# Performance work log

Hardware: AMD Instinct MI355X
Metric: run time of the kernel (lower is better)

Reference implementation:

```python
import jax, jax.numpy as jnp
import numpy as np

NUM_NODES = 50000
NUM_EDGES = 800000
NUM_GRAPHS = 100
NODES_PER_GRAPH = 500
K = 250  # ceil(0.5 * NODES_PER_GRAPH), TopKPooling ratio=0.5
D = 64
OUT = 10


def gcn_conv(x, edge_index, W, b, num_nodes):
    """PyG GCNConv: add self-loops, symmetric D^-1/2 (A+I) D^-1/2 (x @ W) + b."""
    h = x @ W  # [N, Dout]
    loop = jnp.arange(num_nodes)
    row = jnp.concatenate([edge_index[0], loop])  # sources
    col = jnp.concatenate([edge_index[1], loop])  # targets
    deg = jax.ops.segment_sum(jnp.ones_like(col, dtype=h.dtype), col,
                              num_segments=num_nodes)
    dis = jnp.where(deg > 0, jax.lax.rsqrt(jnp.maximum(deg, 1e-12)), 0.0)
    norm = dis[row] * dis[col]                      # [E+N]
    msgs = h[row] * norm[:, None]                   # gather + scale (memory bound)
    out = jax.ops.segment_sum(msgs, col, num_segments=num_nodes)
    return out + b


def setup_inputs() -> dict:
    key = jax.random.key(0)
    ks = jax.random.split(key, 8)
    x = jax.random.normal(ks[0], (NUM_NODES, D), jnp.float32)
    edge_index = jax.random.randint(ks[1], (2, NUM_EDGES), 0, NUM_NODES)
    batch = jnp.arange(NUM_NODES) // NODES_PER_GRAPH  # contiguous equal graphs
    s = 1.0 / np.sqrt(D)
    W0 = jax.random.uniform(ks[2], (D, D), jnp.float32, -s, s)
    b0 = jnp.zeros((D,), jnp.float32)
    W1 = jax.random.uniform(ks[3], (D, D), jnp.float32, -s, s)
    b1 = jnp.zeros((D,), jnp.float32)
    pool_w = jax.random.uniform(ks[4], (D,), jnp.float32, -s, s)
    W_lin = jax.random.uniform(ks[5], (D, OUT), jnp.float32, -s, s)
    b_lin = jnp.zeros((OUT,), jnp.float32)
    return {"x": x, "edge_index": edge_index, "batch": batch,
            "W0": W0, "b0": b0, "W1": W1, "b1": b1,
            "pool_w": pool_w, "W_lin": W_lin, "b_lin": b_lin}


def reference(x, edge_index, batch, W0, b0, W1, b1, pool_w, W_lin, b_lin):
    # NOTE: zip(convs, pools) runs only 2 iterations -> 2 convs, 1 pool.
    x = jax.nn.relu(gcn_conv(x, edge_index, W0, b0, NUM_NODES))
    x = jax.nn.relu(gcn_conv(x, edge_index, W1, b1, NUM_NODES))
    # TopKPooling: score = tanh((x . w) / ||w||), keep top-K per graph,
    # kept features are scaled by their score.
    score = jnp.tanh((x @ pool_w) / jnp.linalg.norm(pool_w))  # [N]
    score_g = score.reshape(NUM_GRAPHS, NODES_PER_GRAPH)
    top_s, top_i = jax.lax.top_k(score_g, K)                  # [G, K]
    gidx = (top_i + jnp.arange(NUM_GRAPHS)[:, None] * NODES_PER_GRAPH).reshape(-1)
    x_pool = x[gidx] * top_s.reshape(-1, 1)                   # [G*K, D]
    # global_mean_pool: each pooled graph has exactly K nodes
    pooled = x_pool.reshape(NUM_GRAPHS, K, D).mean(axis=1)    # [G, D]
    logits = pooled @ W_lin + b_lin                           # [G, OUT]
    return jax.nn.log_softmax(logits, axis=1)
```

## Files before the change

### kernel.cpp

```cpp
#include <hip/hip_runtime.h>
#include <hip/hip_bf16.h>
#include <math.h>

#define NODES 50000
#define EDGES 800000
#define GRAPHS 100
#define NPG 500
#define KTOP 250
#define DIM 64
#define OUTC 10
#define SLOTS 64
#define GROWS 32
#define NBKT 196
#define BCAP 5120

#define WS_FLAG      0u
#define WS_INVNORM   4u
#define WS_W1F       512u
#define WS_B0F       16896u
#define WS_B1F       17152u
#define WS_PWF       17408u
#define WS_WLF       17664u
#define WS_BLF       20224u
#define WS_CURS      20480u
#define WS_CNT       21504u
#define WS_DIS       221696u
#define WS_SCORE     421888u
#define WS_EBUF      622080u
#define WS_SLOT      4636160u
#define WS_H1B       11036160u
#define WS_H2B       17436160u
#define WS_X2        23836160u

__device__ __forceinline__ float bf16_bits_to_f32(unsigned short u) {
    return __uint_as_float(((unsigned int)u) << 16);
}
__device__ __forceinline__ float bf16_lo(unsigned int u) {
    return __uint_as_float(u << 16);
}
__device__ __forceinline__ float bf16_hi(unsigned int u) {
    return __uint_as_float(u & 0xffff0000u);
}
__device__ __forceinline__ unsigned short f32_to_bf16(float f) {
    unsigned int u = __float_as_uint(f);
    u += 0x7fffu + ((u >> 16) & 1u);
    return (unsigned short)(u >> 16);
}
__device__ __forceinline__ unsigned int f32_sortable(float f) {
    unsigned int b = __float_as_uint(f);
    return (b & 0x80000000u) ? ~b : (b | 0x80000000u);
}

__global__ __launch_bounds__(512) void k_bucket(const int* __restrict__ ei,
        const void* w0p, const void* b0p, const void* w1p, const void* b1p,
        const void* pwp, const void* wlp, const void* blp, char* __restrict__ ws) {
    int bid = blockIdx.x, t = threadIdx.x;
    if (bid < NBKT) {
        __shared__ int hist[NBKT];
        __shared__ int base[NBKT];
        if (t < NBKT) hist[t] = 0;
        __syncthreads();
        int e0 = bid * 4096;
        int rr[8], cc[8], loc[8];
        long be = (long)e0 + (long)t * 8;
        if (be + 8 <= EDGES) {
            int4 ra = ((const int4*)(ei + e0))[t * 2];
            int4 rb = ((const int4*)(ei + e0))[t * 2 + 1];
            int4 ca = ((const int4*)(ei + EDGES + e0))[t * 2];
            int4 cb = ((const int4*)(ei + EDGES + e0))[t * 2 + 1];
            rr[0] = ra.x; rr[1] = ra.y; rr[2] = ra.z; rr[3] = ra.w;
            rr[4] = rb.x; rr[5] = rb.y; rr[6] = rb.z; rr[7] = rb.w;
            cc[0] = ca.x; cc[1] = ca.y; cc[2] = ca.z; cc[3] = ca.w;
            cc[4] = cb.x; cc[5] = cb.y; cc[6] = cb.z; cc[7] = cb.w;
        } else {
#pragma unroll
            for (int j = 0; j < 8; j++) {
                long e = be + j;
                if (e < EDGES) { rr[j] = ei[e]; cc[j] = ei[EDGES + e]; }
                else cc[j] = -1;
            }
        }
#pragma unroll
        for (int j = 0; j < 8; j++)
            if (cc[j] >= 0) loc[j] = atomicAdd(&hist[cc[j] >> 8], 1);
        __syncthreads();
        if (t < NBKT) base[t] = atomicAdd((int*)(ws + WS_CURS) + t, hist[t]);
        __syncthreads();
        unsigned int* eb = (unsigned int*)(ws + WS_EBUF);
#pragma unroll
        for (int j = 0; j < 8; j++) {
            if (cc[j] >= 0) {
                int b = cc[j] >> 8;
                int o = base[b] + loc[j];
                if (o < BCAP)
                    eb[b * BCAP + o] =
                        ((unsigned int)(cc[j] & 255) << 16) | (unsigned int)rr[j];
            }
        }
        return;
    }
    __shared__ int red_sh[512];
    __shared__ float fred[64];
    const unsigned short* u16 = (const unsigned short*)w0p;
    int c = 0;
    for (int i = t; i < 4096; i += 512) {
        float v = bf16_bits_to_f32(u16[i]);
        float av = fabsf(v);
        if (v == 0.0f || (av >= 1e-9f && av <= 0.25f)) c++;
    }
    red_sh[t] = c;
    __syncthreads();
    for (int s = 256; s > 0; s >>= 1) {
        if (t < s) red_sh[t] += red_sh[t + s];
        __syncthreads();
    }
    int flag = (red_sh[0] >= 3686) ? 1 : 0;
    if (t == 0) *(int*)(ws + WS_FLAG) = flag;
    const void* srcs[6] = {w1p, b0p, b1p, pwp, wlp, blp};
    const int   ns[6]   = {4096, 64, 64, 64, 640, 10};
    const unsigned int dsts[6] = {WS_W1F, WS_B0F, WS_B1F, WS_PWF, WS_WLF, WS_BLF};
    for (int a = 0; a < 6; a++) {
        float* dst = (float*)(ws + dsts[a]);
        if (flag) {
            const unsigned short* sp = (const unsigned short*)srcs[a];
            for (int i = t; i < ns[a]; i += 512) dst[i] = bf16_bits_to_f32(sp[i]);
        } else {
            const float* sp = (const float*)srcs[a];
            for (int i = t; i < ns[a]; i += 512) dst[i] = sp[i];
        }
    }
    __syncthreads();
    if (t < 64) {
        float w = ((float*)(ws + WS_PWF))[t];
        fred[t] = w * w;
    }
    __syncthreads();
    if (t == 0) {
        float ssum = 0.f;
        for (int i = 0; i < 64; i++) ssum += fred[i];
        *(float*)(ws + WS_INVNORM) = rsqrtf(ssum);
    }
}

__global__ __launch_bounds__(1024) void k_build(char* __restrict__ ws) {
    __shared__ unsigned short slsh[256 * SLOTS];
    __shared__ int cl_cnt[256];
    int b = blockIdx.x, t = threadIdx.x;
    if (t < 256) cl_cnt[t] = 0;
    __syncthreads();
    int n = ((const int*)(ws + WS_CURS))[b];
    if (n > BCAP) n = BCAP;
    const unsigned int* eb = (const unsigned int*)(ws + WS_EBUF) + b * BCAP;
    for (int i = t; i < n; i += 1024) {
        unsigned int u = eb[i];
        int cl = u >> 16;
        int r = u & 0xffffu;
        int p = atomicAdd(&cl_cnt[cl], 1);
        if (p < SLOTS) slsh[cl * SLOTS + p] = (unsigned short)r;
    }
    __syncthreads();
    uint4* dstv = (uint4*)((unsigned short*)(ws + WS_SLOT) + (b << 8) * SLOTS);
    const uint4* srcv = (const uint4*)slsh;
    for (int i = t; i < 2048; i += 1024) dstv[i] = srcv[i];
    if (t < 256) {
        int v = (b << 8) + t;
        if (v < NODES) {
            int cv = cl_cnt[t];
            ((int*)(ws + WS_CNT))[v] = cv;
            ((float*)(ws + WS_DIS))[v] = rsqrtf((float)(cv + 1));
        }
    }
}

__global__ __launch_bounds__(256) void k_gemm0(const void* __restrict__ xp,
        const void* __restrict__ w0p, char* __restrict__ ws,
        unsigned short* __restrict__ H1B) {
    __shared__ float Wsh[64 * 64];
    __shared__ float xsh[GROWS * 65];
    int bid = blockIdx.x, t = threadIdx.x;
    int flag = *(const int*)(ws + WS_FLAG);
    if (flag) {
        const unsigned short* wp = (const unsigned short*)w0p;
        for (int i = t; i < 4096; i += 256) Wsh[i] = bf16_bits_to_f32(wp[i]);
    } else {
        for (int i = t; i < 1024; i += 256)
            ((float4*)Wsh)[i] = ((const float4*)w0p)[i];
    }
    int row0 = bid * GROWS;
    for (int i = t; i < GROWS * 16; i += 256) {
        int r = i >> 4, q = i & 15;
        int gr = row0 + r;
        float4 v = {0.f, 0.f, 0.f, 0.f};
        if (gr < NODES) {
            if (flag) {
                ushort4 u = ((const ushort4*)xp)[gr * 16 + q];
                v.x = bf16_bits_to_f32(u.x); v.y = bf16_bits_to_f32(u.y);
                v.z = bf16_bits_to_f32(u.z); v.w = bf16_bits_to_f32(u.w);
            } else {
                v = ((const float4*)xp)[gr * 16 + q];
            }
        }
        float* xd = xsh + r * 65 + q * 4;
        xd[0] = v.x; xd[1] = v.y; xd[2] = v.z; xd[3] = v.w;
    }
    __syncthreads();
    int tc = t & 15, tr = t >> 4;
    int c0 = tc * 4, r0 = tr * 2;
    float4 a0 = {0, 0, 0, 0}, a1 = {0, 0, 0, 0};
#pragma unroll
    for (int k = 0; k < 64; k++) {
        float4 wv = *(const float4*)(Wsh + k * 64 + c0);
        float x0 = xsh[r0 * 65 + k];
        float x1 = xsh[(r0 + 1) * 65 + k];
        a0.x += wv.x * x0; a0.y += wv.y * x0; a0.z += wv.z * x0; a0.w += wv.w * x0;
        a1.x += wv.x * x1; a1.y += wv.y * x1; a1.z += wv.z * x1; a1.w += wv.w * x1;
    }
    int gr0 = row0 + r0;
    const float* dis = (const float*)(ws + WS_DIS);
    if (gr0 < NODES) {
        float d0 = dis[gr0];
        ushort4 s0;
        s0.x = f32_to_bf16(a0.x * d0); s0.y = f32_to_bf16(a0.y * d0);
        s0.z = f32_to_bf16(a0.z * d0); s0.w = f32_to_bf16(a0.w * d0);
        *(ushort4*)(H1B + gr0 * 64 + c0) = s0;
    }
    if (gr0 + 1 < NODES) {
        float d1 = dis[gr0 + 1];
        ushort4 s1;
        s1.x = f32_to_bf16(a1.x * d1); s1.y = f32_to_bf16(a1.y * d1);
        s1.z = f32_to_bf16(a1.z * d1); s1.w = f32_to_bf16(a1.w * d1);
        *(ushort4*)(H1B + (gr0 + 1) * 64 + c0) = s1;
    }
}

__device__ __forceinline__ void agg_core(const unsigned short* __restrict__ HB,
        const char* __restrict__ ws, int v, int eg, int dh,
        const float* bias, float4& olo, float4& ohi, float& dvo) {
    const int* cnt = (const int*)(ws + WS_CNT);
    const unsigned short* slot = (const unsigned short*)(ws + WS_SLOT) + v * SLOTS;
    const float* dis = (const float*)(ws + WS_DIS);
    int deg = cnt[v];
    if (deg > SLOTS) deg = SLOTS;
    float dv = dis[v];
    dvo = dv;
    float4 alo = {0, 0, 0, 0}, ahi = {0, 0, 0, 0};
    float4 blo = {0, 0, 0, 0}, bhi = {0, 0, 0, 0};
    if (eg == 0) {
        uint4 u = *(const uint4*)(HB + v * 64 + dh * 8);
        alo.x = bf16_lo(u.x); alo.y = bf16_hi(u.x);
        alo.z = bf16_lo(u.y); alo.w = bf16_hi(u.y);
        ahi.x = bf16_lo(u.z); ahi.y = bf16_hi(u.z);
        ahi.z = bf16_lo(u.w); ahi.w = bf16_hi(u.w);
    }
    int e = eg;
    for (; e + 8 < deg; e += 16) {
        int sA = slot[e], sB = slot[e + 8];
        uint4 uA = *(const uint4*)(HB + sA * 64 + dh * 8);
        uint4 uB = *(const uint4*)(HB + sB * 64 + dh * 8);
        alo.x += bf16_lo(uA.x); alo.y += bf16_hi(uA.x);
        alo.z += bf16_lo(uA.y); alo.w += bf16_hi(uA.y);
        ahi.x += bf16_lo(uA.z); ahi.y += bf16_hi(uA.z);
        ahi.z += bf16_lo(uA.w); ahi.w += bf16_hi(uA.w);
        blo.x += bf16_lo(uB.x); blo.y += bf16_hi(uB.x);
        blo.z += bf16_lo(uB.y); blo.w += bf16_hi(uB.y);
        bhi.x += bf16_lo(uB.z); bhi.y += bf16_hi(uB.z);
        bhi.z += bf16_lo(uB.w); bhi.w += bf16_hi(uB.w);
    }
    if (e < deg) {
        int sA = slot[e];
        uint4 uA = *(const uint4*)(HB + sA * 64 + dh * 8);
        alo.x += bf16_lo(uA.x); alo.y += bf16_hi(uA.x);
        alo.z += bf16_lo(uA.y); alo.w += bf16_hi(uA.y);
        ahi.x += bf16_lo(uA.z); ahi.y += bf16_hi(uA.z);
        ahi.z += bf16_lo(uA.w); ahi.w += bf16_hi(uA.w);
    }
    alo.x += blo.x; alo.y += blo.y; alo.z += blo.z; alo.w += blo.w;
    ahi.x += bhi.x; ahi.y += bhi.y; ahi.z += bhi.z; ahi.w += bhi.w;
#pragma unroll
    for (int m = 8; m <= 32; m <<= 1) {
        alo.x += __shfl_xor(alo.x, m, 64); alo.y += __shfl_xor(alo.y, m, 64);
        alo.z += __shfl_xor(alo.z, m, 64); alo.w += __shfl_xor(alo.w, m, 64);
        ahi.x += __shfl_xor(ahi.x, m, 64); ahi.y += __shfl_xor(ahi.y, m, 64);
        ahi.z += __shfl_xor(ahi.z, m, 64); ahi.w += __shfl_xor(ahi.w, m, 64);
    }
    float4 b4a = *(const float4*)(bias + dh * 8);
    float4 b4b = *(const float4*)(bias + dh * 8 + 4);
    olo.x = fmaxf(alo.x * dv + b4a.x, 0.f);
    olo.y = fmaxf(alo.y * dv + b4a.y, 0.f);
    olo.z = fmaxf(alo.z * dv + b4a.z, 0.f);
    olo.w = fmaxf(alo.w * dv + b4a.w, 0.f);
    ohi.x = fmaxf(ahi.x * dv + b4b.x, 0.f);
    ohi.y = fmaxf(ahi.y * dv + b4b.y, 0.f);
    ohi.z = fmaxf(ahi.z * dv + b4b.z, 0.f);
    ohi.w = fmaxf(ahi.w * dv + b4b.w, 0.f);
}

__global__ __launch_bounds__(512) void k_agg1g(const unsigned short* __restrict__ H1B,
        char* __restrict__ ws, unsigned short* __restrict__ H2B) {
    __shared__ float Wsh[4096];
    int t = threadIdx.x;
    const float* W1F = (const float*)(ws + WS_W1F);
    for (int i = t; i < 4096; i += 512) {
        int k = i >> 6, cc = i & 63;
        int qp = (cc >> 2) ^ (k >> 3);
        Wsh[k * 64 + (qp << 2) + (cc & 3)] = W1F[i];
    }
    __syncthreads();
    int wv = t >> 6, lane = t & 63, eg = lane >> 3, dh = lane & 7;
    int v = blockIdx.x * 8 + wv;
    float4 olo, ohi;
    float dv;
    agg_core(H1B, ws, v, eg, dh, (const float*)(ws + WS_B0F), olo, ohi, dv);
    float av[8] = {olo.x, olo.y, olo.z, olo.w, ohi.x, ohi.y, ohi.z, ohi.w};
    float y[8] = {0.f, 0.f, 0.f, 0.f, 0.f, 0.f, 0.f, 0.f};
    const float* Wk = Wsh + dh * 512;
    int q0 = (((eg << 1)) ^ dh) << 2;
    int q1 = (((eg << 1) | 1) ^ dh) << 2;
#pragma unroll
    for (int j = 0; j < 8; j++) {
        float a = av[j];
        float4 w0 = *(const float4*)(Wk + j * 64 + q0);
        float4 w1 = *(const float4*)(Wk + j * 64 + q1);
        y[0] += a * w0.x; y[1] += a * w0.y; y[2] += a * w0.z; y[3] += a * w0.w;
        y[4] += a * w1.x; y[5] += a * w1.y; y[6] += a * w1.z; y[7] += a * w1.w;
    }
#pragma unroll
    for (int m = 1; m <= 4; m <<= 1) {
#pragma unroll
        for (int q = 0; q < 8; q++) y[q] += __shfl_xor(y[q], m, 64);
    }
    if (dh < 2) {
        ushort4 s;
        if (dh == 0) {
            s.x = f32_to_bf16(y[0] * dv); s.y = f32_to_bf16(y[1] * dv);
            s.z = f32_to_bf16(y[2] * dv); s.w = f32_to_bf16(y[3] * dv);
        } else {
            s.x = f32_to_bf16(y[4] * dv); s.y = f32_to_bf16(y[5] * dv);
            s.z = f32_to_bf16(y[6] * dv); s.w = f32_to_bf16(y[7] * dv);
        }
        *(ushort4*)(H2B + v * 64 + (eg << 3) + (dh << 2)) = s;
    }
}

__global__ __launch_bounds__(256) void k_agg_sc(const unsigned short* __restrict__ H2B,
        char* __restrict__ ws, float* __restrict__ X2) {
    int t = threadIdx.x;
    int wv = t >> 6, lane = t & 63, eg = lane >> 3, dh = lane & 7;
    int v = blockIdx.x * 4 + wv;
    float4 olo, ohi;
    float dv;
    agg_core(H2B, ws, v, eg, dh, (const float*)(ws + WS_B1F), olo, ohi, dv);
    if (lane < 8) {
        *(float4*)(X2 + v * 64 + lane * 8) = olo;
        *(float4*)(X2 + v * 64 + lane * 8 + 4) = ohi;
    }
    const float* pw = (const float*)(ws + WS_PWF);
    float4 p4a = *(const float4*)(pw + dh * 8);
    float4 p4b = *(const float4*)(pw + dh * 8 + 4);
    float p = olo.x * p4a.x + olo.y * p4a.y + olo.z * p4a.z + olo.w * p4a.w
            + ohi.x * p4b.x + ohi.y * p4b.y + ohi.z * p4b.z + ohi.w * p4b.w;
    p += __shfl_xor(p, 1, 64);
    p += __shfl_xor(p, 2, 64);
    p += __shfl_xor(p, 4, 64);
    if (lane == 0) {
        float invn = *(const float*)(ws + WS_INVNORM);
        ((float*)(ws + WS_SCORE))[v] = tanhf(p * invn);
    }
}

template<int K, int J>
__device__ __forceinline__ void bstage(unsigned long long (&a)[8], int lane) {
    if constexpr (J >= 8) {
        constexpr int m = J >> 3;
#pragma unroll
        for (int s = 0; s < 8; s++) {
            unsigned long long other = __shfl_xor(a[s], m, 64);
            int e = (lane << 3) | s;
            bool keep_min = ((e & K) == 0) ^ ((lane & m) != 0);
            bool less = a[s] < other;
            a[s] = (keep_min == less) ? a[s] : other;
        }
    } else {
#pragma unroll
        for (int s = 0; s < 8; s++) {
            if ((s & J) == 0) {
                constexpr int j = J;
                int sp = s | j;
                int e = (lane << 3) | s;
                bool up = ((e & K) == 0);
                bool sw = up ? (a[s] > a[sp]) : (a[s] < a[sp]);
                if (sw) { unsigned long long tmp = a[s]; a[s] = a[sp]; a[sp] = tmp; }
            }
        }
    }
    if constexpr (J > 1) bstage<K, (J >> 1)>(a, lane);
}

__global__ __launch_bounds__(256) void k_topk(char* __restrict__ ws,
        const float* __restrict__ X2, void* __restrict__ out) {
    __shared__ unsigned long long pairs[KTOP];
    __shared__ float part[256];
    __shared__ float pool_sh[64];
    __shared__ float lsh[OUTC];
    int g = blockIdx.x, t = threadIdx.x;
    int wv = t >> 6, lane = t & 63;
    const float* sc = (const float*)(ws + WS_SCORE) + g * NPG;

    if (wv == 0) {
        unsigned long long a[8];
#pragma unroll
        for (int s = 0; s < 8; s++) {
            int e = (lane << 3) | s;
            if (e < NPG) {
                unsigned int key = ~f32_sortable(sc[e]);
                a[s] = ((unsigned long long)key << 32) | (unsigned int)e;
            } else {
                a[s] = 0xFFFFFFFFFFFFFFFFull;
            }
        }
        bstage<2, 1>(a, lane);
        bstage<4, 2>(a, lane);
        bstage<8, 4>(a, lane);
        bstage<16, 8>(a, lane);
        bstage<32, 16>(a, lane);
        bstage<64, 32>(a, lane);
        bstage<128, 64>(a, lane);
        bstage<256, 128>(a, lane);
        bstage<512, 256>(a, lane);
#pragma unroll
        for (int s = 0; s < 8; s++) {
            int r = (lane << 3) | s;
            if (r < KTOP) pairs[r] = a[s];
        }
    }
    __syncthreads();

    int d = lane;
    float acc = 0.f;
    for (int r = wv; r < KTOP; r += 4) {
        unsigned long long p = pairs[r];
        unsigned int u = ~(unsigned int)(p >> 32);
        unsigned int sbits = (u & 0x80000000u) ? (u ^ 0x80000000u) : ~u;
        float score = __uint_as_float(sbits);
        int idx = (int)(p & 0xFFFFFFFFu);
        acc += score * X2[(g * NPG + idx) * 64 + d];
    }
    part[t] = acc;
    __syncthreads();
    if (wv == 0)
        pool_sh[d] = (part[d] + part[64 + d] + part[128 + d] + part[192 + d]) * (1.0f / KTOP);
    __syncthreads();
    if (t < 64) {
        float pd = pool_sh[t];
        const float* Wl = (const float*)(ws + WS_WLF);
        const float* bl = (const float*)(ws + WS_BLF);
        for (int o = 0; o < OUTC; o++) {
            float p = pd * Wl[t * OUTC + o];
            for (int s = 32; s > 0; s >>= 1) p += __shfl_down(p, s, 64);
            if (t == 0) lsh[o] = p + bl[o];
        }
        if (t == 0) {
            int flag = *(const int*)(ws + WS_FLAG);
            float mx = lsh[0];
            for (int o = 1; o < OUTC; o++) mx = fmaxf(mx, lsh[o]);
            float se = 0.f;
            for (int o = 0; o < OUTC; o++) se += expf(lsh[o] - mx);
            float lse = logf(se);
            for (int o = 0; o < OUTC; o++) {
                float vv = lsh[o] - mx - lse;
                if (flag) ((__hip_bfloat16*)out)[g * OUTC + o] = __float2bfloat16(vv);
                else      ((float*)out)[g * OUTC + o] = vv;
            }
        }
    }
}

extern "C" void kernel_launch(void* const* d_in, const int* in_sizes, int n_in,
                              void* d_out, int out_size, void* d_ws, size_t ws_size,
                              hipStream_t stream) {
    (void)in_sizes; (void)n_in; (void)out_size; (void)ws_size;
    char* ws = (char*)d_ws;
    const void* xp = d_in[0];
    const int* ei = (const int*)d_in[1];
    unsigned short* H1B = (unsigned short*)(ws + WS_H1B);
    unsigned short* H2B = (unsigned short*)(ws + WS_H2B);
    float* X2 = (float*)(ws + WS_X2);

    (void)hipMemsetAsync(ws + WS_CURS, 0, NBKT * sizeof(int), stream);
    k_bucket<<<NBKT + 1, 512, 0, stream>>>(ei, d_in[3], d_in[4], d_in[5],
                                           d_in[6], d_in[7], d_in[8], d_in[9], ws);
    k_build<<<NBKT, 1024, 0, stream>>>(ws);
    k_gemm0<<<1563, 256, 0, stream>>>(xp, d_in[3], ws, H1B);
    k_agg1g<<<6250, 512, 0, stream>>>(H1B, ws, H2B);
    k_agg_sc<<<12500, 256, 0, stream>>>(H2B, ws, X2);
    k_topk<<<100, 256, 0, stream>>>(ws, X2, d_out);
}
```

Baseline: 158.3 us.

## Remap second aggregation to eight threads per node with serial edge loop

The second GCN aggregation kernel is rewritten so that each node is handled by 8 lanes, each owning 8 feature columns, instead of a full 64-lane wavefront. Each lane walks the node's neighbor slot list sequentially, two edges at a time with dual accumulators. This drops the cross-lane shuffle reductions and the idle lanes of the old per-wave scheme. In exchange each thread runs a serial dependent loop over up to 64 neighbors, so memory-level parallelism per node falls and load imbalance from varying degrees grows.

Measured after the change: 152.1 us. -3.9%, faster.

```diff
diff --git a/kernel.cpp b/kernel.cpp
--- a/kernel.cpp
+++ b/kernel.cpp
@@ -342,27 +342,69 @@
     }
 }
 
-__global__ __launch_bounds__(256) void k_agg_sc(const unsigned short* __restrict__ H2B,
+__global__ __launch_bounds__(256) void k_agg2(const unsigned short* __restrict__ H2B,
         char* __restrict__ ws, float* __restrict__ X2) {
     int t = threadIdx.x;
-    int wv = t >> 6, lane = t & 63, eg = lane >> 3, dh = lane & 7;
-    int v = blockIdx.x * 4 + wv;
-    float4 olo, ohi;
-    float dv;
-    agg_core(H2B, ws, v, eg, dh, (const float*)(ws + WS_B1F), olo, ohi, dv);
-    if (lane < 8) {
-        *(float4*)(X2 + v * 64 + lane * 8) = olo;
-        *(float4*)(X2 + v * 64 + lane * 8 + 4) = ohi;
-    }
-    const float* pw = (const float*)(ws + WS_PWF);
-    float4 p4a = *(const float4*)(pw + dh * 8);
-    float4 p4b = *(const float4*)(pw + dh * 8 + 4);
-    float p = olo.x * p4a.x + olo.y * p4a.y + olo.z * p4a.z + olo.w * p4a.w
-            + ohi.x * p4b.x + ohi.y * p4b.y + ohi.z * p4b.z + ohi.w * p4b.w;
+    int g = t >> 3, dl = t & 7;
+    int v = blockIdx.x * 32 + g;
+    if (v >= NODES) return;
+    int deg = ((const int*)(ws + WS_CNT))[v];
+    if (deg > SLOTS) deg = SLOTS;
+    float dv = ((const float*)(ws + WS_DIS))[v];
+    const unsigned short* slot = (const unsigned short*)(ws + WS_SLOT) + v * SLOTS;
+    const unsigned short* rb = H2B + dl * 8;
+    uint4 u = *(const uint4*)(rb + v * 64);
+    float a0 = bf16_lo(u.x), a1 = bf16_hi(u.x), a2 = bf16_lo(u.y), a3 = bf16_hi(u.y);
+    float a4 = bf16_lo(u.z), a5 = bf16_hi(u.z), a6 = bf16_lo(u.w), a7 = bf16_hi(u.w);
+    float b0 = 0.f, b1 = 0.f, b2 = 0.f, b3 = 0.f;
+    float b4 = 0.f, b5 = 0.f, b6 = 0.f, b7 = 0.f;
+    int e = 0;
+    for (; e + 1 < deg; e += 2) {
+        int sA = slot[e], sB = slot[e + 1];
+        uint4 uA = *(const uint4*)(rb + sA * 64);
+        uint4 uB = *(const uint4*)(rb + sB * 64);
+        a0 += bf16_lo(uA.x); a1 += bf16_hi(uA.x);
+        a2 += bf16_lo(uA.y); a3 += bf16_hi(uA.y);
+        a4 += bf16_lo(uA.z); a5 += bf16_hi(uA.z);
+        a6 += bf16_lo(uA.w); a7 += bf16_hi(uA.w);
+        b0 += bf16_lo(uB.x); b1 += bf16_hi(uB.x);
+        b2 += bf16_lo(uB.y); b3 += bf16_hi(uB.y);
+        b4 += bf16_lo(uB.z); b5 += bf16_hi(uB.z);
+        b6 += bf16_lo(uB.w); b7 += bf16_hi(uB.w);
+    }
+    if (e < deg) {
+        int sA = slot[e];
+        uint4 uA = *(const uint4*)(rb + sA * 64);
+        a0 += bf16_lo(uA.x); a1 += bf16_hi(uA.x);
+        a2 += bf16_lo(uA.y); a3 += bf16_hi(uA.y);
+        a4 += bf16_lo(uA.z); a5 += bf16_hi(uA.z);
+        a6 += bf16_lo(uA.w); a7 += bf16_hi(uA.w);
+    }
+    a0 += b0; a1 += b1; a2 += b2; a3 += b3;
+    a4 += b4; a5 += b5; a6 += b6; a7 += b7;
+    const float* bias = (const float*)(ws + WS_B1F) + dl * 8;
+    float4 bb0 = *(const float4*)(bias);
+    float4 bb1 = *(const float4*)(bias + 4);
+    float4 o0, o1;
+    o0.x = fmaxf(a0 * dv + bb0.x, 0.f);
+    o0.y = fmaxf(a1 * dv + bb0.y, 0.f);
+    o0.z = fmaxf(a2 * dv + bb0.z, 0.f);
+    o0.w = fmaxf(a3 * dv + bb0.w, 0.f);
+    o1.x = fmaxf(a4 * dv + bb1.x, 0.f);
+    o1.y = fmaxf(a5 * dv + bb1.y, 0.f);
+    o1.z = fmaxf(a6 * dv + bb1.z, 0.f);
+    o1.w = fmaxf(a7 * dv + bb1.w, 0.f);
+    *(float4*)(X2 + v * 64 + dl * 8) = o0;
+    *(float4*)(X2 + v * 64 + dl * 8 + 4) = o1;
+    const float* pw = (const float*)(ws + WS_PWF) + dl * 8;
+    float4 pa = *(const float4*)(pw);
+    float4 pb = *(const float4*)(pw + 4);
+    float p = o0.x * pa.x + o0.y * pa.y + o0.z * pa.z + o0.w * pa.w
+            + o1.x * pb.x + o1.y * pb.y + o1.z * pb.z + o1.w * pb.w;
     p += __shfl_xor(p, 1, 64);
     p += __shfl_xor(p, 2, 64);
     p += __shfl_xor(p, 4, 64);
-    if (lane == 0) {
+    if (dl == 0) {
         float invn = *(const float*)(ws + WS_INVNORM);
         ((float*)(ws + WS_SCORE))[v] = tanhf(p * invn);
     }
@@ -492,6 +534,6 @@
     k_build<<<NBKT, 1024, 0, stream>>>(ws);
     k_gemm0<<<1563, 256, 0, stream>>>(xp, d_in[3], ws, H1B);
     k_agg1g<<<6250, 512, 0, stream>>>(H1B, ws, H2B);
-    k_agg_sc<<<12500, 256, 0, stream>>>(H2B, ws, X2);
+    k_agg2<<<1563, 256, 0, stream>>>(H2B, ws, X2);
     k_topk<<<100, 256, 0, stream>>>(ws, X2, d_out);
 }
```

## Split feature halves into separate buffers and aggregate each half in its own pass

Applied to the files above, without the earlier changes.

Node feature tables are stored as two 32-column bf16 halves, and each GCN aggregation runs as two launches, one per half. The goal is a smaller gather working set per pass so it fits better in cache. The second layer's transform, previously fused into the first aggregation, becomes a separate GEMM kernel over an intermediate bf16 activation buffer. The score dot product is split across the halves, with the partial sum kept in scratch. The cost is more launches and an extra write and read of the intermediate activations.

New measurement: 173.1 us. 9.4% more time.

```diff
diff --git a/kernel.cpp b/kernel.cpp
--- a/kernel.cpp
+++ b/kernel.cpp
@@ -13,6 +13,9 @@
 #define GROWS 32
 #define NBKT 196
 #define BCAP 5120
+
+typedef unsigned int nuint4 __attribute__((ext_vector_type(4)));
+typedef float nfloat4 __attribute__((ext_vector_type(4)));
 
 #define WS_FLAG      0u
 #define WS_INVNORM   4u
@@ -28,9 +31,14 @@
 #define WS_SCORE     421888u
 #define WS_EBUF      622080u
 #define WS_SLOT      4636160u
-#define WS_H1B       11036160u
-#define WS_H2B       17436160u
+#define WS_H1LO      11036160u
+#define WS_H1HI      14236160u
+#define WS_H2LO      17436160u
+#define WS_H2HI      20636160u
 #define WS_X2        23836160u
+#define WS_A1LO      WS_X2
+#define WS_A1HI      27036160u
+#define WS_PLO       WS_EBUF
 
 __device__ __forceinline__ float bf16_bits_to_f32(unsigned short u) {
     return __uint_as_float(((unsigned int)u) << 16);
@@ -46,9 +54,18 @@
     u += 0x7fffu + ((u >> 16) & 1u);
     return (unsigned short)(u >> 16);
 }
+__device__ __forceinline__ unsigned int pack_bf16x2(float lo, float hi) {
+    return ((unsigned int)f32_to_bf16(hi) << 16) | (unsigned int)f32_to_bf16(lo);
+}
 __device__ __forceinline__ unsigned int f32_sortable(float f) {
     unsigned int b = __float_as_uint(f);
     return (b & 0x80000000u) ? ~b : (b | 0x80000000u);
+}
+__device__ __forceinline__ void acc8(const uint4& u, float* a) {
+    a[0] += bf16_lo(u.x); a[1] += bf16_hi(u.x);
+    a[2] += bf16_lo(u.y); a[3] += bf16_hi(u.y);
+    a[4] += bf16_lo(u.z); a[5] += bf16_hi(u.z);
+    a[6] += bf16_lo(u.w); a[7] += bf16_hi(u.w);
 }
 
 __global__ __launch_bounds__(512) void k_bucket(const int* __restrict__ ei,
@@ -174,7 +191,7 @@
 
 __global__ __launch_bounds__(256) void k_gemm0(const void* __restrict__ xp,
         const void* __restrict__ w0p, char* __restrict__ ws,
-        unsigned short* __restrict__ H1B) {
+        unsigned short* __restrict__ H1LO, unsigned short* __restrict__ H1HI) {
     __shared__ float Wsh[64 * 64];
     __shared__ float xsh[GROWS * 65];
     int bid = blockIdx.x, t = threadIdx.x;
@@ -222,149 +239,184 @@
         ushort4 s0;
         s0.x = f32_to_bf16(a0.x * d0); s0.y = f32_to_bf16(a0.y * d0);
         s0.z = f32_to_bf16(a0.z * d0); s0.w = f32_to_bf16(a0.w * d0);
-        *(ushort4*)(H1B + gr0 * 64 + c0) = s0;
+        unsigned short* dst = (c0 < 32) ? (H1LO + gr0 * 32 + c0)
+                                        : (H1HI + gr0 * 32 + (c0 - 32));
+        *(ushort4*)dst = s0;
     }
     if (gr0 + 1 < NODES) {
         float d1 = dis[gr0 + 1];
         ushort4 s1;
         s1.x = f32_to_bf16(a1.x * d1); s1.y = f32_to_bf16(a1.y * d1);
         s1.z = f32_to_bf16(a1.z * d1); s1.w = f32_to_bf16(a1.w * d1);
-        *(ushort4*)(H1B + (gr0 + 1) * 64 + c0) = s1;
-    }
-}
-
-__device__ __forceinline__ void agg_core(const unsigned short* __restrict__ HB,
-        const char* __restrict__ ws, int v, int eg, int dh,
-        const float* bias, float4& olo, float4& ohi, float& dvo) {
-    const int* cnt = (const int*)(ws + WS_CNT);
+        unsigned short* dst = (c0 < 32) ? (H1LO + (gr0 + 1) * 32 + c0)
+                                        : (H1HI + (gr0 + 1) * 32 + (c0 - 32));
+        *(ushort4*)dst = s1;
+    }
+}
+
+__global__ __launch_bounds__(256) void k_agg1h(const unsigned short* __restrict__ Hh,
+        char* __restrict__ ws, unsigned short* __restrict__ A1h, int half) {
+    int t = threadIdx.x;
+    int g = t >> 3, l8 = t & 7, eg = l8 >> 2, dl = l8 & 3;
+    int v = blockIdx.x * 32 + g;
+    if (v >= NODES) return;
+    int deg = ((const int*)(ws + WS_CNT))[v];
+    if (deg > SLOTS) deg = SLOTS;
+    float dv = ((const float*)(ws + WS_DIS))[v];
     const unsigned short* slot = (const unsigned short*)(ws + WS_SLOT) + v * SLOTS;
+    const unsigned short* rb = Hh + dl * 8;
+    float a[8] = {0, 0, 0, 0, 0, 0, 0, 0};
+    float b[8] = {0, 0, 0, 0, 0, 0, 0, 0};
+    if (eg == 0) {
+        uint4 u = *(const uint4*)(rb + v * 32);
+        acc8(u, a);
+    }
+    int e = eg;
+    for (; e + 2 < deg; e += 4) {
+        int sA = slot[e], sB = slot[e + 2];
+        uint4 uA = *(const uint4*)(rb + sA * 32);
+        uint4 uB = *(const uint4*)(rb + sB * 32);
+        acc8(uA, a); acc8(uB, b);
+    }
+    if (e < deg) {
+        uint4 uA = *(const uint4*)(rb + slot[e] * 32);
+        acc8(uA, a);
+    }
+#pragma unroll
+    for (int j = 0; j < 8; j++) {
+        a[j] += b[j];
+        a[j] += __shfl_xor(a[j], 4, 64);
+    }
+    const float* bias = (const float*)(ws + WS_B0F) + half * 32 + dl * 8;
+    float o[8];
+#pragma unroll
+    for (int j = 0; j < 8; j++) o[j] = fmaxf(a[j] * dv + bias[j], 0.f);
+    if (eg == 0) {
+        nuint4 s;
+        s.x = pack_bf16x2(o[0], o[1]); s.y = pack_bf16x2(o[2], o[3]);
+        s.z = pack_bf16x2(o[4], o[5]); s.w = pack_bf16x2(o[6], o[7]);
+        __builtin_nontemporal_store(s, (nuint4*)(A1h + v * 32 + dl * 8));
+    }
+}
+
+__global__ __launch_bounds__(256) void k_gemm1(char* __restrict__ ws,
+        unsigned short* __restrict__ H2LO, unsigned short* __restrict__ H2HI) {
+    __shared__ float Wsh[64 * 64];
+    __shared__ float xsh[GROWS * 65];
+    int bid = blockIdx.x, t = threadIdx.x;
+    const float* W1F = (const float*)(ws + WS_W1F);
+    for (int i = t; i < 1024; i += 256)
+        ((float4*)Wsh)[i] = ((const float4*)W1F)[i];
+    const unsigned short* A1LO = (const unsigned short*)(ws + WS_A1LO);
+    const unsigned short* A1HI = (const unsigned short*)(ws + WS_A1HI);
+    int row0 = bid * GROWS;
+    for (int i = t; i < GROWS * 16; i += 256) {
+        int r = i >> 4, q = i & 15;
+        int gr = row0 + r;
+        int cc = q * 4;
+        float4 vv = {0.f, 0.f, 0.f, 0.f};
+        if (gr < NODES) {
+            const unsigned short* src = (cc < 32) ? (A1LO + gr * 32 + cc)
+                                                  : (A1HI + gr * 32 + (cc - 32));
+            ushort4 u = *(const ushort4*)src;
+            vv.x = bf16_bits_to_f32(u.x); vv.y = bf16_bits_to_f32(u.y);
+            vv.z = bf16_bits_to_f32(u.z); vv.w = bf16_bits_to_f32(u.w);
+        }
+        float* xd = xsh + r * 65 + cc;
+        xd[0] = vv.x; xd[1] = vv.y; xd[2] = vv.z; xd[3] = vv.w;
+    }
+    __syncthreads();
+    int tc = t & 15, tr = t >> 4;
+    int c0 = tc * 4, r0 = tr * 2;
+    float4 a0 = {0, 0, 0, 0}, a1 = {0, 0, 0, 0};
+#pragma unroll
+    for (int k = 0; k < 64; k++) {
+        float4 wv = *(const float4*)(Wsh + k * 64 + c0);
+        float x0 = xsh[r0 * 65 + k];
+        float x1 = xsh[(r0 + 1) * 65 + k];
+        a0.x += wv.x * x0; a0.y += wv.y * x0; a0.z += wv.z * x0; a0.w += wv.w * x0;
+        a1.x += wv.x * x1; a1.y += wv.y * x1; a1.z += wv.z * x1; a1.w += wv.w * x1;
+    }
+    int gr0 = row0 + r0;
     const float* dis = (const float*)(ws + WS_DIS);
-    int deg = cnt[v];
+    if (gr0 < NODES) {
+        float d = dis[gr0];
+        ushort4 s;
+        s.x = f32_to_bf16(a0.x * d); s.y = f32_to_bf16(a0.y * d);
+        s.z = f32_to_bf16(a0.z * d); s.w = f32_to_bf16(a0.w * d);
+        unsigned short* dst = (c0 < 32) ? (H2LO + gr0 * 32 + c0)
+                                        : (H2HI + gr0 * 32 + (c0 - 32));
+        *(ushort4*)dst = s;
+    }
+    if (gr0 + 1 < NODES) {
+        float d = dis[gr0 + 1];
+        ushort4 s;
+        s.x = f32_to_bf16(a1.x * d); s.y = f32_to_bf16(a1.y * d);
+        s.z = f32_to_bf16(a1.z * d); s.w = f32_to_bf16(a1.w * d);
+        unsigned short* dst = (c0 < 32) ? (H2LO + (gr0 + 1) * 32 + c0)
+                                        : (H2HI + (gr0 + 1) * 32 + (c0 - 32));
+        *(ushort4*)dst = s;
+    }
+}
+
+__global__ __launch_bounds__(256) void k_agg2h(const unsigned short* __restrict__ Hh,
+        char* __restrict__ ws, float* __restrict__ X2, int half) {
+    int t = threadIdx.x;
+    int g = t >> 3, l8 = t & 7, eg = l8 >> 2, dl = l8 & 3;
+    int v = blockIdx.x * 32 + g;
+    if (v >= NODES) return;
+    int deg = ((const int*)(ws + WS_CNT))[v];
     if (deg > SLOTS) deg = SLOTS;
-    float dv = dis[v];
-    dvo = dv;
-    float4 alo = {0, 0, 0, 0}, ahi = {0, 0, 0, 0};
-    float4 blo = {0, 0, 0, 0}, bhi = {0, 0, 0, 0};
+    float dv = ((const float*)(ws + WS_DIS))[v];
+    const unsigned short* slot = (const unsigned short*)(ws + WS_SLOT) + v * SLOTS;
+    const unsigned short* rb = Hh + dl * 8;
+    float a[8] = {0, 0, 0, 0, 0, 0, 0, 0};
+    float b[8] = {0, 0, 0, 0, 0, 0, 0, 0};
     if (eg == 0) {
-        uint4 u = *(const uint4*)(HB + v * 64 + dh * 8);
-        alo.x = bf16_lo(u.x); alo.y = bf16_hi(u.x);
-        alo.z = bf16_lo(u.y); alo.w = bf16_hi(u.y);
-        ahi.x = bf16_lo(u.z); ahi.y = bf16_hi(u.z);
-        ahi.z = bf16_lo(u.w); ahi.w = bf16_hi(u.w);
+        uint4 u = *(const uint4*)(rb + v * 32);
+        acc8(u, a);
     }
     int e = eg;
-    for (; e + 8 < deg; e += 16) {
-        int sA = slot[e], sB = slot[e + 8];
-        uint4 uA = *(const uint4*)(HB + sA * 64 + dh * 8);
-        uint4 uB = *(const uint4*)(HB + sB * 64 + dh * 8);
-        alo.x += bf16_lo(uA.x); alo.y += bf16_hi(uA.x);
-        alo.z += bf16_lo(uA.y); alo.w += bf16_hi(uA.y);
-        ahi.x += bf16_lo(uA.z); ahi.y += bf16_hi(uA.z);
-        ahi.z += bf16_lo(uA.w); ahi.w += bf16_hi(uA.w);
-        blo.x += bf16_lo(uB.x); blo.y += bf16_hi(uB.x);
-        blo.z += bf16_lo(uB.y); blo.w += bf16_hi(uB.y);
-        bhi.x += bf16_lo(uB.z); bhi.y += bf16_hi(uB.z);
-        bhi.z += bf16_lo(uB.w); bhi.w += bf16_hi(uB.w);
+    for (; e + 2 < deg; e += 4) {
+        int sA = slot[e], sB = slot[e + 2];
+        uint4 uA = *(const uint4*)(rb + sA * 32);
+        uint4 uB = *(const uint4*)(rb + sB * 32);
+        acc8(uA, a); acc8(uB, b);
     }
     if (e < deg) {
-        int sA = slot[e];
-        uint4 uA = *(const uint4*)(HB + sA * 64 + dh * 8);
-        alo.x += bf16_lo(uA.x); alo.y += bf16_hi(uA.x);
-        alo.z += bf16_lo(uA.y); alo.w += bf16_hi(uA.y);
-        ahi.x += bf16_lo(uA.z); ahi.y += bf16_hi(uA.z);
-        ahi.z += bf16_lo(uA.w); ahi.w += bf16_hi(uA.w);
-    }
-    alo.x += blo.x; alo.y += blo.y; alo.z += blo.z; alo.w += blo.w;
-    ahi.x += bhi.x; ahi.y += bhi.y; ahi.z += bhi.z; ahi.w += bhi.w;
-#pragma unroll
-    for (int m = 8; m <= 32; m <<= 1) {
-        alo.x += __shfl_xor(alo.x, m, 64); alo.y += __shfl_xor(alo.y, m, 64);
-        alo.z += __shfl_xor(alo.z, m, 64); alo.w += __shfl_xor(alo.w, m, 64);
-        ahi.x += __shfl_xor(ahi.x, m, 64); ahi.y += __shfl_xor(ahi.y, m, 64);
-        ahi.z += __shfl_xor(ahi.z, m, 64); ahi.w += __shfl_xor(ahi.w, m, 64);
-    }
-    float4 b4a = *(const float4*)(bias + dh * 8);
-    float4 b4b = *(const float4*)(bias + dh * 8 + 4);
-    olo.x = fmaxf(alo.x * dv + b4a.x, 0.f);
-    olo.y = fmaxf(alo.y * dv + b4a.y, 0.f);
-    olo.z = fmaxf(alo.z * dv + b4a.z, 0.f);
-    olo.w = fmaxf(alo.w * dv + b4a.w, 0.f);
-    ohi.x = fmaxf(ahi.x * dv + b4b.x, 0.f);
-    ohi.y = fmaxf(ahi.y * dv + b4b.y, 0.f);
-    ohi.z = fmaxf(ahi.z * dv + b4b.z, 0.f);
-    ohi.w = fmaxf(ahi.w * dv + b4b.w, 0.f);
-}
-
-__global__ __launch_bounds__(512) void k_agg1g(const unsigned short* __restrict__ H1B,
-        char* __restrict__ ws, unsigned short* __restrict__ H2B) {
-    __shared__ float Wsh[4096];
-    int t = threadIdx.x;
-    const float* W1F = (const float*)(ws + WS_W1F);
-    for (int i = t; i < 4096; i += 512) {
-        int k = i >> 6, cc = i & 63;
-        int qp = (cc >> 2) ^ (k >> 3);
-        Wsh[k * 64 + (qp << 2) + (cc & 3)] = W1F[i];
-    }
-    __syncthreads();
-    int wv = t >> 6, lane = t & 63, eg = lane >> 3, dh = lane & 7;
-    int v = blockIdx.x * 8 + wv;
-    float4 olo, ohi;
-    float dv;
-    agg_core(H1B, ws, v, eg, dh, (const float*)(ws + WS_B0F), olo, ohi, dv);
-    float av[8] = {olo.x, olo.y, olo.z, olo.w, ohi.x, ohi.y, ohi.z, ohi.w};
-    float y[8] = {0.f, 0.f, 0.f, 0.f, 0.f, 0.f, 0.f, 0.f};
-    const float* Wk = Wsh + dh * 512;
-    int q0 = (((eg << 1)) ^ dh) << 2;
-    int q1 = (((eg << 1) | 1) ^ dh) << 2;
+        uint4 uA = *(const uint4*)(rb + slot[e] * 32);
+        acc8(uA, a);
+    }
 #pragma unroll
     for (int j = 0; j < 8; j++) {
-        float a = av[j];
-        float4 w0 = *(const float4*)(Wk + j * 64 + q0);
-        float4 w1 = *(const float4*)(Wk + j * 64 + q1);
-        y[0] += a * w0.x; y[1] += a * w0.y; y[2] += a * w0.z; y[3] += a * w0.w;
-        y[4] += a * w1.x; y[5] += a * w1.y; y[6] += a * w1.z; y[7] += a * w1.w;
-    }
-#pragma unroll
-    for (int m = 1; m <= 4; m <<= 1) {
-#pragma unroll
-        for (int q = 0; q < 8; q++) y[q] += __shfl_xor(y[q], m, 64);
-    }
-    if (dh < 2) {
-        ushort4 s;
-        if (dh == 0) {
-            s.x = f32_to_bf16(y[0] * dv); s.y = f32_to_bf16(y[1] * dv);
-            s.z = f32_to_bf16(y[2] * dv); s.w = f32_to_bf16(y[3] * dv);
-        } else {
-            s.x = f32_to_bf16(y[4] * dv); s.y = f32_to_bf16(y[5] * dv);
-            s.z = f32_to_bf16(y[6] * dv); s.w = f32_to_bf16(y[7] * dv);
-        }
-        *(ushort4*)(H2B + v * 64 + (eg << 3) + (dh << 2)) = s;
-    }
-}
-
-__global__ __launch_bounds__(256) void k_agg_sc(const unsigned short* __restrict__ H2B,
-        char* __restrict__ ws, float* __restrict__ X2) {
-    int t = threadIdx.x;
-    int wv = t >> 6, lane = t & 63, eg = lane >> 3, dh = lane & 7;
-    int v = blockIdx.x * 4 + wv;
-    float4 olo, ohi;
-    float dv;
-    agg_core(H2B, ws, v, eg, dh, (const float*)(ws + WS_B1F), olo, ohi, dv);
-    if (lane < 8) {
-        *(float4*)(X2 + v * 64 + lane * 8) = olo;
-        *(float4*)(X2 + v * 64 + lane * 8 + 4) = ohi;
-    }
-    const float* pw = (const float*)(ws + WS_PWF);
-    float4 p4a = *(const float4*)(pw + dh * 8);
-    float4 p4b = *(const float4*)(pw + dh * 8 + 4);
-    float p = olo.x * p4a.x + olo.y * p4a.y + olo.z * p4a.z + olo.w * p4a.w
-            + ohi.x * p4b.x + ohi.y * p4b.y + ohi.z * p4b.z + ohi.w * p4b.w;
+        a[j] += b[j];
+        a[j] += __shfl_xor(a[j], 4, 64);
+    }
+    const float* bias = (const float*)(ws + WS_B1F) + half * 32 + dl * 8;
+    float o[8];
+#pragma unroll
+    for (int j = 0; j < 8; j++) o[j] = fmaxf(a[j] * dv + bias[j], 0.f);
+    if (eg == 0) {
+        nfloat4 f0 = {o[0], o[1], o[2], o[3]};
+        nfloat4 f1 = {o[4], o[5], o[6], o[7]};
+        float* xb = X2 + v * 64 + half * 32 + dl * 8;
+        __builtin_nontemporal_store(f0, (nfloat4*)xb);
+        __builtin_nontemporal_store(f1, (nfloat4*)(xb + 4));
+    }
+    const float* pw = (const float*)(ws + WS_PWF) + half * 32 + dl * 8;
+    float p = 0.f;
+#pragma unroll
+    for (int j = 0; j < 8; j++) p += o[j] * pw[j];
     p += __shfl_xor(p, 1, 64);
     p += __shfl_xor(p, 2, 64);
-    p += __shfl_xor(p, 4, 64);
-    if (lane == 0) {
-        float invn = *(const float*)(ws + WS_INVNORM);
-        ((float*)(ws + WS_SCORE))[v] = tanhf(p * invn);
+    if (l8 == 0) {
+        float* plo = (float*)(ws + WS_PLO);
+        if (half == 0) {
+            plo[v] = p;
+        } else {
+            float invn = *(const float*)(ws + WS_INVNORM);
+            ((float*)(ws + WS_SCORE))[v] = tanhf((p + plo[v]) * invn);
+        }
     }
 }
 
@@ -482,16 +534,23 @@
     char* ws = (char*)d_ws;
     const void* xp = d_in[0];
     const int* ei = (const int*)d_in[1];
-    unsigned short* H1B = (unsigned short*)(ws + WS_H1B);
-    unsigned short* H2B = (unsigned short*)(ws + WS_H2B);
+    unsigned short* H1LO = (unsigned short*)(ws + WS_H1LO);
+    unsigned short* H1HI = (unsigned short*)(ws + WS_H1HI);
+    unsigned short* H2LO = (unsigned short*)(ws + WS_H2LO);
+    unsigned short* H2HI = (unsigned short*)(ws + WS_H2HI);
+    unsigned short* A1LO = (unsigned short*)(ws + WS_A1LO);
+    unsigned short* A1HI = (unsigned short*)(ws + WS_A1HI);
     float* X2 = (float*)(ws + WS_X2);
 
     (void)hipMemsetAsync(ws + WS_CURS, 0, NBKT * sizeof(int), stream);
     k_bucket<<<NBKT + 1, 512, 0, stream>>>(ei, d_in[3], d_in[4], d_in[5],
                                            d_in[6], d_in[7], d_in[8], d_in[9], ws);
     k_build<<<NBKT, 1024, 0, stream>>>(ws);
-    k_gemm0<<<1563, 256, 0, stream>>>(xp, d_in[3], ws, H1B);
-    k_agg1g<<<6250, 512, 0, stream>>>(H1B, ws, H2B);
-    k_agg_sc<<<12500, 256, 0, stream>>>(H2B, ws, X2);
+    k_gemm0<<<1563, 256, 0, stream>>>(xp, d_in[3], ws, H1LO, H1HI);
+    k_agg1h<<<1563, 256, 0, stream>>>(H1LO, ws, A1LO, 0);
+    k_agg1h<<<1563, 256, 0, stream>>>(H1HI, ws, A1HI, 1);
+    k_gemm1<<<1563, 256, 0, stream>>>(ws, H2LO, H2HI);
+    k_agg2h<<<1563, 256, 0, stream>>>(H2LO, ws, X2, 0);
+    k_agg2h<<<1563, 256, 0, stream>>>(H2HI, ws, X2, 1);
     k_topk<<<100, 256, 0, stream>>>(ws, X2, d_out);
 }
```
